# Performance work log

Measured on AMD Instinct MI355X. Metric: run time of the kernel, lower is better.

The kernel has to match this reference:

```python
import jax, jax.numpy as jnp
import numpy as np

N = 100000   # nodes
E = 1600000  # edges (before self-loops)
IN = 128     # in_num
H1, C1 = 8, 8    # gat1: 8 heads x 8 channels -> 64 concat
OUT = 32     # out_num (gat2: 1 head x 32)


def setup_inputs() -> dict:
    key = jax.random.key(0)
    ks = jax.random.split(key, 10)
    g = lambda k, shape, fan: (jax.random.normal(k, shape, jnp.float32) / np.sqrt(fan).astype(np.float32))
    return {
        "x": jax.random.normal(ks[0], (N, IN), jnp.float32),
        "edge_index": jax.random.randint(ks[1], (2, E), 0, N, dtype=jnp.int64),
        "W1": g(ks[2], (IN, H1 * C1), IN),
        "a_src1": g(ks[3], (H1, C1), C1),
        "a_dst1": g(ks[4], (H1, C1), C1),
        "b1": jnp.zeros((H1 * C1,), jnp.float32),
        "W2": g(ks[5], (H1 * C1, OUT), H1 * C1),
        "a_src2": g(ks[6], (1, OUT), OUT),
        "a_dst2": g(ks[7], (1, OUT), OUT),
        "b2": jnp.zeros((OUT,), jnp.float32),
    }


def _gat_layer(x, src, dst, W, a_src, a_dst, b, heads, ch):
    # PyG GATConv (concat=True, negative_slope=0.2). Dropout (p=0.6) is a
    # no-op in eval mode and omitted.
    n = x.shape[0]
    h = (x @ W).reshape(n, heads, ch)                        # [N,H,C]
    al_s = jnp.einsum('nhc,hc->nh', h, a_src)                # [N,H]
    al_d = jnp.einsum('nhc,hc->nh', h, a_dst)
    e = jax.nn.leaky_relu(al_s[src] + al_d[dst], negative_slope=0.2)  # [E,H]
    # segment softmax over incoming edges of each dst node
    m = jax.lax.stop_gradient(jax.ops.segment_max(e, dst, num_segments=n))
    ex = jnp.exp(e - m[dst])
    denom = jax.ops.segment_sum(ex, dst, num_segments=n)
    alpha = ex / denom[dst]                                  # [E,H]
    out = jax.ops.segment_sum(h[src] * alpha[:, :, None], dst, num_segments=n)
    return out.reshape(n, heads * ch) + b


def reference(x, edge_index, W1, a_src1, a_dst1, b1, W2, a_src2, a_dst2, b2):
    loop = jnp.arange(N, dtype=edge_index.dtype)
    src = jnp.concatenate([edge_index[0], loop])  # add_self_loops=True (PyG default)
    dst = jnp.concatenate([edge_index[1], loop])
    h = _gat_layer(x, src, dst, W1, a_src1, a_dst1, b1, H1, C1)   # [N,64]
    out = _gat_layer(h, src, dst, W2, a_src2, a_dst2, b2, 1, OUT)  # [N,OUT]
    return out
```

## Files before the change

### kernel.cpp

```cpp
#include <hip/hip_runtime.h>
#include <hip/hip_bf16.h>


#define SLAB  4096
#define NBUCK 512

typedef float v2f __attribute__((ext_vector_type(2)));

__device__ __forceinline__ float lrelu02(float x) { return x > 0.f ? x : 0.2f * x; }

__device__ __forceinline__ unsigned short f2bf(float v) {
    __hip_bfloat16 b = __float2bfloat16(v);
    return __builtin_bit_cast(unsigned short, b);
}

__device__ __forceinline__ void accum8(uint4 hv, float ex, v2f* acc) {
    v2f ex2 = {ex, ex};
#pragma unroll
    for (int q = 0; q < 4; ++q) {
        unsigned u = (&hv.x)[q];
        v2f h2 = {__uint_as_float(u << 16), __uint_as_float(u & 0xffff0000u)};
        acc[q] = __builtin_elementwise_fma(h2, ex2, acc[q]);
    }
}

__device__ __forceinline__ v2f shfl_xor_v2(v2f v, int mask) {
    v2f r;
    r.x = __shfl_xor(v.x, mask, 64);
    r.y = __shfl_xor(v.y, mask, 64);
    return r;
}

__device__ __forceinline__ void scatter_body(char* smem, int vbid,
                                             const int* __restrict__ ei,
                                             int e_real, int e_total, unsigned M,
                                             int* __restrict__ bcur_pad,
                                             int2* __restrict__ pairs) {
    int*  cnt   = (int*)smem;
    int*  loff  = cnt + 512;
    int*  lcur  = loff + 512;
    int*  gbase = lcur + 512;
    int2* stag  = (int2*)(gbase + 512);
    unsigned short* bb = (unsigned short*)(stag + 4096);

    const int t = threadIdx.x;
    const int base = vbid * 4096;
    cnt[t] = 0; cnt[t + 256] = 0;
    __syncthreads();

    int rs[16], rd[16], rb[16];
#pragma unroll
    for (int k = 0; k < 16; ++k) {
        int i = base + k * 256 + t;
        bool val = i < e_total;
        int s = 0, d = 0;
        if (val) {
            if (i < e_real) { s = ei[i]; d = ei[e_real + i]; }
            else            { s = d = i - e_real; }
        }
        int b = val ? (int)__umulhi((unsigned)d, M) : -1;
        rs[k] = s; rd[k] = d; rb[k] = b;
        if (val) atomicAdd(&cnt[b], 1);
    }
    __syncthreads();

    loff[t] = cnt[t]; loff[t + 256] = cnt[t + 256];
    __syncthreads();
    for (int off = 1; off < 512; off <<= 1) {
        int v0 = (t >= off) ? loff[t - off] : 0;
        int v1 = (t + 256 >= off) ? loff[t + 256 - off] : 0;
        __syncthreads();
        loff[t] += v0; loff[t + 256] += v1;
        __syncthreads();
    }
    int e0 = loff[t] - cnt[t];
    int e1 = loff[t + 256] - cnt[t + 256];
    loff[t] = e0;           loff[t + 256] = e1;
    lcur[t] = e0;           lcur[t + 256] = e1;
    gbase[t]       = t * SLAB         + atomicAdd(&bcur_pad[t * 16], cnt[t]);
    gbase[t + 256] = (t + 256) * SLAB + atomicAdd(&bcur_pad[(t + 256) * 16],
                                                  cnt[t + 256]);
    __syncthreads();

#pragma unroll
    for (int k = 0; k < 16; ++k) {
        if (rb[k] >= 0) {
            int lp = atomicAdd(&lcur[rb[k]], 1);
            stag[lp] = make_int2(rs[k], rd[k]);
            bb[lp]   = (unsigned short)rb[k];
        }
    }
    __syncthreads();

    int cn = e_total - base; if (cn > 4096) cn = 4096;
    for (int idx = t; idx < cn; idx += 256) {
        int b = bb[idx];
        int g = gbase[b] + (idx - loff[b]);
        pairs[g] = stag[idx];
    }
}

template<int K, int OUTC, int H, int C, int NPT, int KCHUNK>
__device__ __forceinline__ void gemm_al_body(char* smem, int vbid,
                                             const float* __restrict__ x,
                                             const float* __restrict__ W,
                                             const float* __restrict__ a_src,
                                             const float* __restrict__ a_dst,
                                             unsigned short* __restrict__ h,
                                             float* __restrict__ al_s,
                                             float* __restrict__ al_d,
                                             int n) {
    constexpr int COLG = OUTC / 4;
    constexpr int NG   = 256 / COLG;
    static_assert(NG * 8 == NPT, "tile mismatch");
    constexpr int LDX  = KCHUNK + 1;
    float* Xs = (float*)smem;
    float* Ws = Xs + NPT * LDX;

    const int t    = threadIdx.x;
    const int mg   = t / COLG;
    const int cg   = t % COLG;
    const int base = vbid * NPT;

    float acc[8][4];
#pragma unroll
    for (int i = 0; i < 8; ++i)
#pragma unroll
        for (int j = 0; j < 4; ++j) acc[i][j] = 0.f;

    for (int kc = 0; kc < K; kc += KCHUNK) {
        __syncthreads();
        constexpr int F4R = KCHUNK / 4;
        constexpr int TOTF4 = NPT * F4R;
#pragma unroll
        for (int r = 0; r < TOTF4 / 256; ++r) {
            int f4   = r * 256 + t;
            int node = f4 / F4R;
            int kq   = f4 % F4R;
            int gn   = base + node; if (gn > n - 1) gn = n - 1;
            const float4 v = *(const float4*)&x[(size_t)gn * K + kc + kq * 4];
            float* d = &Xs[node * LDX + kq * 4];
            d[0] = v.x; d[1] = v.y; d[2] = v.z; d[3] = v.w;
        }
        constexpr int WF4 = KCHUNK * OUTC / 4;
        for (int idx = t; idx < WF4; idx += 256)
            *(float4*)&Ws[idx * 4] = *(const float4*)&W[(size_t)kc * OUTC + idx * 4];
        __syncthreads();

#pragma unroll 4
        for (int k = 0; k < KCHUNK; ++k) {
            float4 b = *(const float4*)&Ws[k * OUTC + cg * 4];
            float a[8];
#pragma unroll
            for (int i = 0; i < 8; ++i) a[i] = Xs[(mg * 8 + i) * LDX + k];
#pragma unroll
            for (int i = 0; i < 8; ++i) {
                acc[i][0] += a[i] * b.x;
                acc[i][1] += a[i] * b.y;
                acc[i][2] += a[i] * b.z;
                acc[i][3] += a[i] * b.w;
            }
        }
    }

    const float4 as4 = *(const float4*)&a_src[cg * 4];
    const float4 ad4 = *(const float4*)&a_dst[cg * 4];
    constexpr int GPH = C / 4;
    const int head = cg / GPH;
#pragma unroll
    for (int i = 0; i < 8; ++i) {
        int gn = base + mg * 8 + i;
        bool ok = gn < n;
        if (ok) {
            ushort4 hv;
            hv.x = f2bf(acc[i][0]); hv.y = f2bf(acc[i][1]);
            hv.z = f2bf(acc[i][2]); hv.w = f2bf(acc[i][3]);
            *(ushort4*)&h[(size_t)gn * OUTC + cg * 4] = hv;
        }
        float ps = acc[i][0] * as4.x + acc[i][1] * as4.y +
                   acc[i][2] * as4.z + acc[i][3] * as4.w;
        float pd = acc[i][0] * ad4.x + acc[i][1] * ad4.y +
                   acc[i][2] * ad4.z + acc[i][3] * ad4.w;
#pragma unroll
        for (int s = 1; s < GPH; s <<= 1) {
            ps += __shfl_xor(ps, s, 64);
            pd += __shfl_xor(pd, s, 64);
        }
        if (ok && (cg % GPH) == 0) {
            al_s[(size_t)gn * H + head] = ps;
            al_d[(size_t)gn * H + head] = pd;
        }
    }
}

__global__ __launch_bounds__(256)
void scatter_gemm_kernel(const int* __restrict__ ei, int e_real, int e_total,
                         unsigned M, int* __restrict__ bcur_pad,
                         int2* __restrict__ pairs, int ns,
                         const float* __restrict__ x,
                         const float* __restrict__ W1,
                         const float* __restrict__ as1,
                         const float* __restrict__ ad1,
                         unsigned short* __restrict__ h,
                         float* __restrict__ al_s,
                         float* __restrict__ al_d, int n) {
    __shared__ __align__(16) char smem[49664];
    if ((int)blockIdx.x < ns)
        scatter_body(smem, blockIdx.x, ei, e_real, e_total, M, bcur_pad, pairs);
    else
        gemm_al_body<128, 64, 8, 8, 128, 64>(smem, blockIdx.x - ns,
                                             x, W1, as1, ad1, h, al_s, al_d, n);
}

template<int K, int OUTC, int H, int C, int NPT, int KCHUNK>
__global__ __launch_bounds__(256)
void gemm_al_kernel(const float* __restrict__ x, const float* __restrict__ W,
                    const float* __restrict__ a_src, const float* __restrict__ a_dst,
                    unsigned short* __restrict__ h, float* __restrict__ al_s,
                    float* __restrict__ al_d, int n) {
    __shared__ __align__(16) char smem[(NPT * (KCHUNK + 1) + KCHUNK * OUTC) * 4];
    gemm_al_body<K, OUTC, H, C, NPT, KCHUNK>(smem, blockIdx.x, x, W, a_src,
                                             a_dst, h, al_s, al_d, n);
}

__global__ __launch_bounds__(256)
void csr_finalize_kernel(const int2* __restrict__ pairs,
                         const int* __restrict__ bcur_pad,
                         unsigned M, int n,
                         int* __restrict__ offsets,
                         int* __restrict__ srcs) {
    const int b = blockIdx.x;
    const int t = threadIdx.x;
    const unsigned long long Mll = M;
    int lo = (int)((((unsigned long long)b << 32) + Mll - 1) / Mll);
    int hi = (int)((((unsigned long long)(b + 1) << 32) + Mll - 1) / Mll);
    if (lo > n) lo = n;
    if (hi > n) hi = n;
    const int R    = hi - lo;
    const int cntb = bcur_pad[b * 16];
    const int2* sp = pairs + (size_t)b * SLAB;

    __shared__ int bs[NBUCK];
    __shared__ int ebeg_s;
    bs[t] = bcur_pad[t * 16];
    bs[t + 256] = bcur_pad[(t + 256) * 16];
    __syncthreads();
    for (int off = 1; off < NBUCK; off <<= 1) {
        int v0 = (t >= off) ? bs[t - off] : 0;
        int v1 = (t + 256 >= off) ? bs[t + 256 - off] : 0;
        __syncthreads();
        bs[t] += v0; bs[t + 256] += v1;
        __syncthreads();
    }
    if (t == 0) ebeg_s = (b == 0) ? 0 : bs[b - 1];
    if (b == NBUCK - 1 && t == 0) offsets[n] = bs[NBUCK - 1];
    __syncthreads();
    const int ebeg = ebeg_s;

    __shared__ int deg[256], sc[256], cur[256];
    deg[t] = 0;
    __syncthreads();
    for (int j = t; j < cntb; j += 256)
        atomicAdd(&deg[sp[j].y - lo], 1);
    __syncthreads();

    sc[t] = deg[t];
    __syncthreads();
    for (int off = 1; off < 256; off <<= 1) {
        int v = (t >= off) ? sc[t - off] : 0;
        __syncthreads();
        sc[t] += v;
        __syncthreads();
    }
    int e0 = sc[t] - deg[t];
    cur[t] = e0;
    if (t < R) offsets[lo + t] = ebeg + e0;
    __syncthreads();

    for (int j = t; j < cntb; j += 256) {
        int2 p = sp[j];
        int pos = atomicAdd(&cur[p.y - lo], 1);
        srcs[ebeg + pos] = p.x;
    }
}

template<int H, int C>
__global__ __launch_bounds__(256)
void gat_agg_kernel(const int* __restrict__ offsets,
                    const int* __restrict__ srcs,
                    const float* __restrict__ al_s,
                    const float* __restrict__ al_d,
                    const unsigned short* __restrict__ hfeat,
                    const float* __restrict__ bias,
                    float* __restrict__ out, int n) {
    constexpr int OUTC = H * C;
    constexpr int CG   = OUTC / 8;
    constexpr int ES   = 64 / CG;
    const int wid  = (int)((blockIdx.x * blockDim.x + threadIdx.x) >> 6);
    const int lane = threadIdx.x & 63;
    const int cg   = lane % CG;
    const int es   = lane / CG;
    if (wid >= n) return;
    const int head = (cg * 8) / C;

    const float aldv = al_d[(size_t)wid * H + head];
    const int beg = offsets[wid];
    const int end = offsets[wid + 1];
    const int deg = end - beg;

    v2f acc[4];
#pragma unroll
    for (int q = 0; q < 4; ++q) acc[q] = (v2f){0.f, 0.f};
    float dsum = 0.f;

    if (deg <= ES) {
        int j = beg + es;
        bool v = j < end;
        int s = __builtin_nontemporal_load(&srcs[v ? j : beg]);
        const uint4 hv = *(const uint4*)&hfeat[(size_t)s * OUTC + cg * 8];
        float ls = al_s[(size_t)s * H + head];
        float ex = v ? __expf(lrelu02(ls + aldv)) : 0.f;
        accum8(hv, ex, acc);
        dsum += ex;
    } else if (deg <= 2 * ES) {
        int sA = __builtin_nontemporal_load(&srcs[beg + es]);
        int jB = beg + ES + es;
        bool vB = jB < end;
        int sB = __builtin_nontemporal_load(&srcs[vB ? jB : beg]);
        const uint4 hvA = *(const uint4*)&hfeat[(size_t)sA * OUTC + cg * 8];
        const uint4 hvB = *(const uint4*)&hfeat[(size_t)sB * OUTC + cg * 8];
        float lsA = al_s[(size_t)sA * H + head];
        float lsB = al_s[(size_t)sB * H + head];
        float exA = __expf(lrelu02(lsA + aldv));
        float exB = vB ? __expf(lrelu02(lsB + aldv)) : 0.f;
        accum8(hvA, exA, acc);
        accum8(hvB, exB, acc);
        dsum += exA + exB;
    } else if (deg <= 4 * ES) {
        int sA = __builtin_nontemporal_load(&srcs[beg + es]);
        int sB = __builtin_nontemporal_load(&srcs[beg + ES + es]);
        int jC = beg + 2 * ES + es;
        int jD = beg + 3 * ES + es;
        bool vC = jC < end;
        bool vD = jD < end;
        int sC = __builtin_nontemporal_load(&srcs[vC ? jC : beg]);
        int sD = __builtin_nontemporal_load(&srcs[vD ? jD : beg]);
        const uint4 hvA = *(const uint4*)&hfeat[(size_t)sA * OUTC + cg * 8];
        const uint4 hvB = *(const uint4*)&hfeat[(size_t)sB * OUTC + cg * 8];
        const uint4 hvC = *(const uint4*)&hfeat[(size_t)sC * OUTC + cg * 8];
        const uint4 hvD = *(const uint4*)&hfeat[(size_t)sD * OUTC + cg * 8];
        float lsA = al_s[(size_t)sA * H + head];
        float lsB = al_s[(size_t)sB * H + head];
        float lsC = al_s[(size_t)sC * H + head];
        float lsD = al_s[(size_t)sD * H + head];
        float exA = __expf(lrelu02(lsA + aldv));
        float exB = __expf(lrelu02(lsB + aldv));
        float exC = vC ? __expf(lrelu02(lsC + aldv)) : 0.f;
        float exD = vD ? __expf(lrelu02(lsD + aldv)) : 0.f;
        accum8(hvA, exA, acc);
        accum8(hvB, exB, acc);
        accum8(hvC, exC, acc);
        accum8(hvD, exD, acc);
        dsum += (exA + exB) + (exC + exD);
    } else {
        for (int j0 = beg; j0 < end; j0 += 2 * ES) {
            int jA = j0 + es;
            int jB = j0 + ES + es;
            bool vA = jA < end;
            bool vB = jB < end;
            int sA = __builtin_nontemporal_load(&srcs[vA ? jA : beg]);
            int sB = __builtin_nontemporal_load(&srcs[vB ? jB : beg]);
            const uint4 hvA = *(const uint4*)&hfeat[(size_t)sA * OUTC + cg * 8];
            const uint4 hvB = *(const uint4*)&hfeat[(size_t)sB * OUTC + cg * 8];
            float lsA = al_s[(size_t)sA * H + head];
            float lsB = al_s[(size_t)sB * H + head];
            float exA = vA ? __expf(lrelu02(lsA + aldv)) : 0.f;
            float exB = vB ? __expf(lrelu02(lsB + aldv)) : 0.f;
            accum8(hvA, exA, acc);
            accum8(hvB, exB, acc);
            dsum += exA + exB;
        }
    }

#pragma unroll
    for (int sh = CG; sh < 64; sh <<= 1) {
        dsum += __shfl_xor(dsum, sh, 64);
#pragma unroll
        for (int q = 0; q < 4; ++q) acc[q] += shfl_xor_v2(acc[q], sh);
    }

    if (es == 0) {
        float inv = 1.f / dsum;
        const float4 b0 = *(const float4*)&bias[cg * 8];
        const float4 b1 = *(const float4*)&bias[cg * 8 + 4];
        float4 o0, o1;
        o0.x = acc[0].x * inv + b0.x;
        o0.y = acc[0].y * inv + b0.y;
        o0.z = acc[1].x * inv + b0.z;
        o0.w = acc[1].y * inv + b0.w;
        o1.x = acc[2].x * inv + b1.x;
        o1.y = acc[2].y * inv + b1.y;
        o1.z = acc[3].x * inv + b1.z;
        o1.w = acc[3].y * inv + b1.w;
        *(float4*)&out[(size_t)wid * OUTC + cg * 8]     = o0;
        *(float4*)&out[(size_t)wid * OUTC + cg * 8 + 4] = o1;
    }
}


extern "C" void kernel_launch(void* const* d_in, const int* in_sizes, int n_in,
                              void* d_out, int out_size, void* d_ws, size_t ws_size,
                              hipStream_t stream) {
    const float* x   = (const float*)d_in[0];
    const int*   ei  = (const int*)  d_in[1];
    const float* W1  = (const float*)d_in[2];
    const float* as1 = (const float*)d_in[3];
    const float* ad1 = (const float*)d_in[4];
    const float* b1  = (const float*)d_in[5];
    const float* W2  = (const float*)d_in[6];
    const float* as2 = (const float*)d_in[7];
    const float* ad2 = (const float*)d_in[8];
    const float* b2  = (const float*)d_in[9];
    float* out = (float*)d_out;

    const int n       = in_sizes[0] / 128;
    const int e_real  = in_sizes[1] / 2;
    const int e_total = e_real + n;
    const unsigned M512 = (unsigned)(((unsigned long long)NBUCK << 32) / (unsigned)n);

    unsigned short* h1u = (unsigned short*)d_ws;
    float* fws  = (float*)d_ws;
    float* als1 = fws  + (size_t)n * 32;
    float* ald1 = als1 + (size_t)n * 8;
    float* agg1 = ald1 + (size_t)n * 8;
    int2*  pairs = (int2*)agg1;
    int* offsets  = (int*)(agg1 + (size_t)n * 64);
    int* srcs     = offsets + (n + 1);
    int* bcur_pad = srcs + e_total;

    const int ns = (e_total + 4095) / 4096;
    const int g1 = (n + 127) / 128;

    hipMemsetAsync(bcur_pad, 0, NBUCK * 16 * sizeof(int), stream);
    scatter_gemm_kernel<<<ns + g1, 256, 0, stream>>>(
        ei, e_real, e_total, M512, bcur_pad, pairs, ns,
        x, W1, as1, ad1, h1u, als1, ald1, n);
    csr_finalize_kernel<<<NBUCK, 256, 0, stream>>>(pairs, bcur_pad, M512, n,
                                                   offsets, srcs);

    gat_agg_kernel<8, 8><<<(n + 3) / 4, 256, 0, stream>>>(
        offsets, srcs, als1, ald1, h1u, b1, agg1, n);

    gemm_al_kernel<64, 32, 1, 32, 256, 32><<<(n + 255) / 256, 256, 0, stream>>>(
        agg1, W2, as2, ad2, h1u, als1, ald1, n);
    gat_agg_kernel<1, 32><<<(n + 3) / 4, 256, 0, stream>>>(
        offsets, srcs, als1, ald1, h1u, b2, out, n);
}
```

Baseline: 270.0 us.

## Fuse layer-1 aggregation with layer-2 GEMM and shrink scatter tiles

The layer-1 GAT aggregation kernel now also runs the layer-2 linear projection and attention logits per node, using a transposed W2 kept in shared memory. This removes the separate GEMM launch and the fp32 round trip of the 64-wide aggregated features through global memory. Separately, the scatter tile drops from 4096 to 2048 edges and the layer-1 GEMM KCHUNK from 64 to 32, which cuts the fused kernel's shared memory from 49664 to 28672 bytes for higher occupancy. The cost is a W2 load into shared memory in every aggregation block plus an extra block barrier, and twice as many scatter blocks.

Result: slower. 310.9 us (+15.1%).

```diff
diff --git a/kernel.cpp b/kernel.cpp
--- a/kernel.cpp
+++ b/kernel.cpp
@@ -40,17 +40,18 @@
     int*  loff  = cnt + 512;
     int*  lcur  = loff + 512;
     int*  gbase = lcur + 512;
-    int2* stag  = (int2*)(gbase + 512);
-    unsigned short* bb = (unsigned short*)(stag + 4096);
+    int*  ssrc  = gbase + 512;
+    int*  sdst  = ssrc + 2048;
+    unsigned short* bb = (unsigned short*)(sdst + 2048);
 
     const int t = threadIdx.x;
-    const int base = vbid * 4096;
+    const int base = vbid * 2048;
     cnt[t] = 0; cnt[t + 256] = 0;
     __syncthreads();
 
-    int rs[16], rd[16], rb[16];
-#pragma unroll
-    for (int k = 0; k < 16; ++k) {
+    int rs[8], rd[8], rb[8];
+#pragma unroll
+    for (int k = 0; k < 8; ++k) {
         int i = base + k * 256 + t;
         bool val = i < e_total;
         int s = 0, d = 0;
@@ -83,20 +84,21 @@
     __syncthreads();
 
 #pragma unroll
-    for (int k = 0; k < 16; ++k) {
+    for (int k = 0; k < 8; ++k) {
         if (rb[k] >= 0) {
             int lp = atomicAdd(&lcur[rb[k]], 1);
-            stag[lp] = make_int2(rs[k], rd[k]);
+            ssrc[lp] = rs[k];
+            sdst[lp] = rd[k];
             bb[lp]   = (unsigned short)rb[k];
         }
     }
     __syncthreads();
 
-    int cn = e_total - base; if (cn > 4096) cn = 4096;
+    int cn = e_total - base; if (cn > 2048) cn = 2048;
     for (int idx = t; idx < cn; idx += 256) {
         int b = bb[idx];
         int g = gbase[b] + (idx - loff[b]);
-        pairs[g] = stag[idx];
+        pairs[g] = make_int2(ssrc[idx], sdst[idx]);
     }
 }
 
@@ -204,23 +206,12 @@
                          unsigned short* __restrict__ h,
                          float* __restrict__ al_s,
                          float* __restrict__ al_d, int n) {
-    __shared__ __align__(16) char smem[49664];
+    __shared__ __align__(16) char smem[28672];
     if ((int)blockIdx.x < ns)
         scatter_body(smem, blockIdx.x, ei, e_real, e_total, M, bcur_pad, pairs);
     else
-        gemm_al_body<128, 64, 8, 8, 128, 64>(smem, blockIdx.x - ns,
+        gemm_al_body<128, 64, 8, 8, 128, 32>(smem, blockIdx.x - ns,
                                              x, W1, as1, ad1, h, al_s, al_d, n);
-}
-
-template<int K, int OUTC, int H, int C, int NPT, int KCHUNK>
-__global__ __launch_bounds__(256)
-void gemm_al_kernel(const float* __restrict__ x, const float* __restrict__ W,
-                    const float* __restrict__ a_src, const float* __restrict__ a_dst,
-                    unsigned short* __restrict__ h, float* __restrict__ al_s,
-                    float* __restrict__ al_d, int n) {
-    __shared__ __align__(16) char smem[(NPT * (KCHUNK + 1) + KCHUNK * OUTC) * 4];
-    gemm_al_body<K, OUTC, H, C, NPT, KCHUNK>(smem, blockIdx.x, x, W, a_src,
-                                             a_dst, h, al_s, al_d, n);
 }
 
 __global__ __launch_bounds__(256)
@@ -284,24 +275,40 @@
     }
 }
 
-template<int H, int C>
 __global__ __launch_bounds__(256)
-void gat_agg_kernel(const int* __restrict__ offsets,
-                    const int* __restrict__ srcs,
-                    const float* __restrict__ al_s,
-                    const float* __restrict__ al_d,
-                    const unsigned short* __restrict__ hfeat,
-                    const float* __restrict__ bias,
-                    float* __restrict__ out, int n) {
-    constexpr int OUTC = H * C;
-    constexpr int CG   = OUTC / 8;
-    constexpr int ES   = 64 / CG;
-    const int wid  = (int)((blockIdx.x * blockDim.x + threadIdx.x) >> 6);
-    const int lane = threadIdx.x & 63;
+void agg_gemm2_kernel(const int* __restrict__ offsets,
+                      const int* __restrict__ srcs,
+                      const float* __restrict__ al_s,
+                      const float* __restrict__ al_d,
+                      const unsigned short* __restrict__ hfeat,
+                      const float* __restrict__ b1,
+                      const float* __restrict__ W2,
+                      const float* __restrict__ as2,
+                      const float* __restrict__ ad2,
+                      unsigned short* __restrict__ h2,
+                      float* __restrict__ als2,
+                      float* __restrict__ ald2, int n) {
+    constexpr int H = 8, OUTC = 64, CG = 8, ES = 8;
+    __shared__ float W2t[32 * 65];
+    __shared__ float rowbuf[4][64];
+    __shared__ float b1s[64], as2s[32], ad2s[32];
+
+    const int t = threadIdx.x;
+    for (int idx = t; idx < 2048; idx += 256) {
+        int k = idx >> 5, j = idx & 31;
+        W2t[j * 65 + k] = W2[idx];
+    }
+    if (t < 64)       b1s[t] = b1[t];
+    else if (t < 96)  as2s[t - 64] = as2[t - 64];
+    else if (t < 128) ad2s[t - 96] = ad2[t - 96];
+    __syncthreads();
+
+    const int wid0 = (int)((blockIdx.x * blockDim.x + t) >> 6);
+    const int wid  = wid0 < n ? wid0 : n - 1;
+    const int lane = t & 63;
     const int cg   = lane % CG;
     const int es   = lane / CG;
-    if (wid >= n) return;
-    const int head = (cg * 8) / C;
+    const int head = cg;
 
     const float aldv = al_d[(size_t)wid * H + head];
     const int beg = offsets[wid];
@@ -389,19 +396,159 @@
         for (int q = 0; q < 4; ++q) acc[q] += shfl_xor_v2(acc[q], sh);
     }
 
+    const int w = t >> 6;
+    if (es == 0) {
+        float inv = 1.f / dsum;
+#pragma unroll
+        for (int q = 0; q < 4; ++q) {
+            rowbuf[w][cg * 8 + 2 * q]     = acc[q].x * inv + b1s[cg * 8 + 2 * q];
+            rowbuf[w][cg * 8 + 2 * q + 1] = acc[q].y * inv + b1s[cg * 8 + 2 * q + 1];
+        }
+    }
+    __syncthreads();
+
+    const int j  = lane & 31;
+    const int kh = (lane >> 5) * 32;
+    float o = 0.f;
+#pragma unroll
+    for (int it = 0; it < 8; ++it) {
+        const float4 r = *(const float4*)&rowbuf[w][kh + it * 4];
+        const float* wp = &W2t[j * 65 + kh + it * 4];
+        o += r.x * wp[0] + r.y * wp[1] + r.z * wp[2] + r.w * wp[3];
+    }
+    o += __shfl_xor(o, 32, 64);
+
+    float ps = o * as2s[j];
+    float pd = o * ad2s[j];
+#pragma unroll
+    for (int s = 1; s < 32; s <<= 1) {
+        ps += __shfl_xor(ps, s, 64);
+        pd += __shfl_xor(pd, s, 64);
+    }
+    if (wid0 < n) {
+        if (lane < 32) h2[(size_t)wid * 32 + j] = f2bf(o);
+        if (lane == 0) { als2[wid] = ps; ald2[wid] = pd; }
+    }
+}
+
+template<int H, int C>
+__global__ __launch_bounds__(256)
+void gat_agg_kernel(const int* __restrict__ offsets,
+                    const int* __restrict__ srcs,
+                    const float* __restrict__ al_s,
+                    const float* __restrict__ al_d,
+                    const unsigned short* __restrict__ hfeat,
+                    const float* __restrict__ bias,
+                    float* __restrict__ out, int n) {
+    constexpr int OUTC = H * C;
+    constexpr int CG   = OUTC / 8;
+    constexpr int ES   = 64 / CG;
+    const int wid  = (int)((blockIdx.x * blockDim.x + threadIdx.x) >> 6);
+    const int lane = threadIdx.x & 63;
+    const int cg   = lane % CG;
+    const int es   = lane / CG;
+    if (wid >= n) return;
+    const int head = (cg * 8) / C;
+
+    const float aldv = al_d[(size_t)wid * H + head];
+    const int beg = offsets[wid];
+    const int end = offsets[wid + 1];
+    const int deg = end - beg;
+
+    v2f acc[4];
+#pragma unroll
+    for (int q = 0; q < 4; ++q) acc[q] = (v2f){0.f, 0.f};
+    float dsum = 0.f;
+
+    if (deg <= ES) {
+        int j = beg + es;
+        bool v = j < end;
+        int s = __builtin_nontemporal_load(&srcs[v ? j : beg]);
+        const uint4 hv = *(const uint4*)&hfeat[(size_t)s * OUTC + cg * 8];
+        float ls = al_s[(size_t)s * H + head];
+        float ex = v ? __expf(lrelu02(ls + aldv)) : 0.f;
+        accum8(hv, ex, acc);
+        dsum += ex;
+    } else if (deg <= 2 * ES) {
+        int sA = __builtin_nontemporal_load(&srcs[beg + es]);
+        int jB = beg + ES + es;
+        bool vB = jB < end;
+        int sB = __builtin_nontemporal_load(&srcs[vB ? jB : beg]);
+        const uint4 hvA = *(const uint4*)&hfeat[(size_t)sA * OUTC + cg * 8];
+        const uint4 hvB = *(const uint4*)&hfeat[(size_t)sB * OUTC + cg * 8];
+        float lsA = al_s[(size_t)sA * H + head];
+        float lsB = al_s[(size_t)sB * H + head];
+        float exA = __expf(lrelu02(lsA + aldv));
+        float exB = vB ? __expf(lrelu02(lsB + aldv)) : 0.f;
+        accum8(hvA, exA, acc);
+        accum8(hvB, exB, acc);
+        dsum += exA + exB;
+    } else if (deg <= 4 * ES) {
+        int sA = __builtin_nontemporal_load(&srcs[beg + es]);
+        int sB = __builtin_nontemporal_load(&srcs[beg + ES + es]);
+        int jC = beg + 2 * ES + es;
+        int jD = beg + 3 * ES + es;
+        bool vC = jC < end;
+        bool vD = jD < end;
+        int sC = __builtin_nontemporal_load(&srcs[vC ? jC : beg]);
+        int sD = __builtin_nontemporal_load(&srcs[vD ? jD : beg]);
+        const uint4 hvA = *(const uint4*)&hfeat[(size_t)sA * OUTC + cg * 8];
+        const uint4 hvB = *(const uint4*)&hfeat[(size_t)sB * OUTC + cg * 8];
+        const uint4 hvC = *(const uint4*)&hfeat[(size_t)sC * OUTC + cg * 8];
+        const uint4 hvD = *(const uint4*)&hfeat[(size_t)sD * OUTC + cg * 8];
+        float lsA = al_s[(size_t)sA * H + head];
+        float lsB = al_s[(size_t)sB * H + head];
+        float lsC = al_s[(size_t)sC * H + head];
+        float lsD = al_s[(size_t)sD * H + head];
+        float exA = __expf(lrelu02(lsA + aldv));
+        float exB = __expf(lrelu02(lsB + aldv));
+        float exC = vC ? __expf(lrelu02(lsC + aldv)) : 0.f;
+        float exD = vD ? __expf(lrelu02(lsD + aldv)) : 0.f;
+        accum8(hvA, exA, acc);
+        accum8(hvB, exB, acc);
+        accum8(hvC, exC, acc);
+        accum8(hvD, exD, acc);
+        dsum += (exA + exB) + (exC + exD);
+    } else {
+        for (int j0 = beg; j0 < end; j0 += 2 * ES) {
+            int jA = j0 + es;
+            int jB = j0 + ES + es;
+            bool vA = jA < end;
+            bool vB = jB < end;
+            int sA = __builtin_nontemporal_load(&srcs[vA ? jA : beg]);
+            int sB = __builtin_nontemporal_load(&srcs[vB ? jB : beg]);
+            const uint4 hvA = *(const uint4*)&hfeat[(size_t)sA * OUTC + cg * 8];
+            const uint4 hvB = *(const uint4*)&hfeat[(size_t)sB * OUTC + cg * 8];
+            float lsA = al_s[(size_t)sA * H + head];
+            float lsB = al_s[(size_t)sB * H + head];
+            float exA = vA ? __expf(lrelu02(lsA + aldv)) : 0.f;
+            float exB = vB ? __expf(lrelu02(lsB + aldv)) : 0.f;
+            accum8(hvA, exA, acc);
+            accum8(hvB, exB, acc);
+            dsum += exA + exB;
+        }
+    }
+
+#pragma unroll
+    for (int sh = CG; sh < 64; sh <<= 1) {
+        dsum += __shfl_xor(dsum, sh, 64);
+#pragma unroll
+        for (int q = 0; q < 4; ++q) acc[q] += shfl_xor_v2(acc[q], sh);
+    }
+
     if (es == 0) {
         float inv = 1.f / dsum;
         const float4 b0 = *(const float4*)&bias[cg * 8];
-        const float4 b1 = *(const float4*)&bias[cg * 8 + 4];
+        const float4 b1v = *(const float4*)&bias[cg * 8 + 4];
         float4 o0, o1;
         o0.x = acc[0].x * inv + b0.x;
         o0.y = acc[0].y * inv + b0.y;
         o0.z = acc[1].x * inv + b0.z;
         o0.w = acc[1].y * inv + b0.w;
-        o1.x = acc[2].x * inv + b1.x;
-        o1.y = acc[2].y * inv + b1.y;
-        o1.z = acc[3].x * inv + b1.z;
-        o1.w = acc[3].y * inv + b1.w;
+        o1.x = acc[2].x * inv + b1v.x;
+        o1.y = acc[2].y * inv + b1v.y;
+        o1.z = acc[3].x * inv + b1v.z;
+        o1.w = acc[3].y * inv + b1v.w;
         *(float4*)&out[(size_t)wid * OUTC + cg * 8]     = o0;
         *(float4*)&out[(size_t)wid * OUTC + cg * 8 + 4] = o1;
     }
@@ -432,13 +579,16 @@
     float* fws  = (float*)d_ws;
     float* als1 = fws  + (size_t)n * 32;
     float* ald1 = als1 + (size_t)n * 8;
-    float* agg1 = ald1 + (size_t)n * 8;
-    int2*  pairs = (int2*)agg1;
-    int* offsets  = (int*)(agg1 + (size_t)n * 64);
+    float* scratch = ald1 + (size_t)n * 8;
+    int2*  pairs = (int2*)scratch;
+    unsigned short* h2 = (unsigned short*)scratch;
+    float* als2 = scratch + (size_t)n * 16;
+    float* ald2 = als2 + n;
+    int* offsets  = (int*)(scratch + (size_t)n * 64);
     int* srcs     = offsets + (n + 1);
     int* bcur_pad = srcs + e_total;
 
-    const int ns = (e_total + 4095) / 4096;
+    const int ns = (e_total + 2047) / 2048;
     const int g1 = (n + 127) / 128;
 
     hipMemsetAsync(bcur_pad, 0, NBUCK * 16 * sizeof(int), stream);
@@ -448,11 +598,9 @@
     csr_finalize_kernel<<<NBUCK, 256, 0, stream>>>(pairs, bcur_pad, M512, n,
                                                    offsets, srcs);
 
-    gat_agg_kernel<8, 8><<<(n + 3) / 4, 256, 0, stream>>>(
-        offsets, srcs, als1, ald1, h1u, b1, agg1, n);
-
-    gemm_al_kernel<64, 32, 1, 32, 256, 32><<<(n + 255) / 256, 256, 0, stream>>>(
-        agg1, W2, as2, ad2, h1u, als1, ald1, n);
+    agg_gemm2_kernel<<<(n + 3) / 4, 256, 0, stream>>>(
+        offsets, srcs, als1, ald1, h1u, b1, W2, as2, ad2, h2, als2, ald2, n);
+
     gat_agg_kernel<1, 32><<<(n + 3) / 4, 256, 0, stream>>>(
-        offsets, srcs, als1, ald1, h1u, b2, out, n);
-}
+        offsets, srcs, als2, ald2, h2, b2, out, n);
+}
```
